# Performance work log

Measured on AMD Instinct MI355X. Metric: run time of the kernel, lower is better.

The kernel has to match this reference:

```python
import jax, jax.numpy as jnp
import numpy as np

N, D_IN, N_CTRS, D_OUT = 65536, 64, 1024, 256


def setup_inputs() -> dict:
    key = jax.random.key(0)
    k_x, k_c, k_v = jax.random.split(key, 3)
    x = jax.random.normal(k_x, (N, D_IN), dtype=jnp.float32)
    # learned params: centers (init_ctrs 'random' draws from data scale), values (normal), scales s=ones
    ctrs = jax.random.normal(k_c, (N_CTRS, D_IN), dtype=jnp.float32)
    values = jax.random.normal(k_v, (N_CTRS, D_OUT), dtype=jnp.float32) * 1e-2
    s = jnp.ones((D_IN,), dtype=jnp.float32)
    return {"x": x, "ctrs": ctrs, "values": values, "s": s}


def reference(x, ctrs, values, s):
    # dist_sq[n,k] = sum_d (x[n,d]-ctrs[k,d])^2 * s[d]
    # expanded to avoid the (N, n_ctrs, d_in) broadcast intermediate:
    x_sq = jnp.einsum('nd,d->n', x * x, s)            # (N,)
    c_sq = jnp.einsum('kd,d->k', ctrs * ctrs, s)      # (K,)
    cross = jnp.einsum('nd,kd->nk', x * s, ctrs)      # (N, K)
    dist_sq = x_sq[:, None] + c_sq[None, :] - 2.0 * cross
    assignments = jax.nn.softmax(-dist_sq, axis=1)    # (N, K)
    return assignments @ values                        # (N, d_out)
```

## Files before the change

### kernel.cpp

```cpp
#include <hip/hip_runtime.h>

typedef _Float16 half_t;
typedef half_t f16x8 __attribute__((ext_vector_type(8)));
typedef float f32x4 __attribute__((ext_vector_type(4)));
typedef unsigned int u32x2 __attribute__((ext_vector_type(2)));

#define LOG2E 1.44269504088896340736f

#define NROWS 65536
#define DIN   64
#define NCTRS 1024
#define DOUT  256

#define CSWZ_OFF 0
#define CSWZ_BYTES (128 * 1024)
#define VSWZ_OFF (CSWZ_OFF + CSWZ_BYTES)
#define VSWZ_BYTES (512 * 1024)
#define CSQ_OFF  (VSWZ_OFF + VSWZ_BYTES)

#define VT_STRIDE 260
#define CT_STRIDE 68

#define RESCALE_THR 8.0f

#define GLOAD_LDS16(g, l)                                                      \
  __builtin_amdgcn_global_load_lds(                                            \
      (const __attribute__((address_space(1))) void*)(const void*)(g),         \
      (__attribute__((address_space(3))) void*)(void*)(l), 16, 0, 0)

__global__ __launch_bounds__(256) void precompute_kernel(
    const float* __restrict__ ctrs, const float* __restrict__ values,
    const float* __restrict__ s, char* __restrict__ ws) {
  half_t* Cswz = (half_t*)(ws + CSWZ_OFF);
  half_t* Vswz = (half_t*)(ws + VSWZ_OFF);
  float* csq2 = (float*)(ws + CSQ_OFF);

  __shared__ half_t Vt[32 * VT_STRIDE];
  __shared__ half_t Ct[32 * CT_STRIDE];

  const int c = blockIdx.x, tid = threadIdx.x;

#pragma unroll
  for (int i = 0; i < 8; ++i) {
    int idx = i * 256 + tid;
    int r = idx >> 6, c4 = (idx & 63) * 4;
    float4 v = ((const float4*)values)[(size_t)(c * 32 + r) * 64 + (idx & 63)];
    Vt[r * VT_STRIDE + c4 + 0] = (half_t)v.x;
    Vt[r * VT_STRIDE + c4 + 1] = (half_t)v.y;
    Vt[r * VT_STRIDE + c4 + 2] = (half_t)v.z;
    Vt[r * VT_STRIDE + c4 + 3] = (half_t)v.w;
  }
#pragma unroll
  for (int i = 0; i < 2; ++i) {
    int idx = i * 256 + tid;
    int r = idx >> 4, c4 = (idx & 15) * 4;
    float4 v = ((const float4*)ctrs)[(size_t)(c * 32 + r) * 16 + (idx & 15)];
    Ct[r * CT_STRIDE + c4 + 0] = (half_t)v.x;
    Ct[r * CT_STRIDE + c4 + 1] = (half_t)v.y;
    Ct[r * CT_STRIDE + c4 + 2] = (half_t)v.z;
    Ct[r * CT_STRIDE + c4 + 3] = (half_t)v.w;
  }
  {
    int k = tid >> 3, dg = (tid & 7) * 8;
    const float* cp = ctrs + (size_t)(c * 32 + k) * DIN + dg;
    float acc = 0.0f;
#pragma unroll
    for (int j = 0; j < 8; ++j) acc = fmaf(cp[j] * cp[j], s[dg + j], acc);
    acc += __shfl_xor(acc, 1);
    acc += __shfl_xor(acc, 2);
    acc += __shfl_xor(acc, 4);
    if ((tid & 7) == 0) csq2[c * 32 + k] = acc * LOG2E;
  }
  __syncthreads();

  const int w = tid >> 6, l = tid & 63, l4 = l >> 4, lm = l & 15;

  {
    int ct = w >> 1, kt = w & 1;
    f16x8 v;
#pragma unroll
    for (int j = 0; j < 8; ++j)
      v[j] = Ct[(ct * 16 + lm) * CT_STRIDE + kt * 32 + l4 * 8 + j];
    *(f16x8*)(Cswz + ((c * 4 + w) * 64 + l) * 8) = v;
  }
#pragma unroll
  for (int q = 0; q < 4; ++q) {
    int sl = w * 4 + q;
    f16x8 v;
#pragma unroll
    for (int j = 0; j < 8; ++j)
      v[j] = Vt[(l4 * 8 + j) * VT_STRIDE + sl * 16 + lm];
    *(f16x8*)(Vswz + ((c * 16 + sl) * 64 + l) * 8) = v;
  }
}

__global__ __launch_bounds__(256, 2) void attn_kernel(
    const float* __restrict__ x, const float* __restrict__ s,
    const char* __restrict__ ws, float* __restrict__ out) {
  const f16x8* cbase = (const f16x8*)(ws + CSWZ_OFF);
  const char* Vraw = ws + VSWZ_OFF;
  const float* csq2 = (const float*)(ws + CSQ_OFF);

  __shared__ __attribute__((aligned(16))) char vbuf[2][16384];

  const int tid = threadIdx.x;
  const int w = tid >> 6, l = tid & 63, l4 = l >> 4, lm = l & 15;
  const int rowbase = blockIdx.x * 128 + w * 32;

#pragma unroll
  for (int i = 0; i < 4; ++i) {
    GLOAD_LDS16(Vraw + i * 4096 + tid * 16, &vbuf[0][i * 4096 + w * 1024]);
  }

  f16x8 A[2][2];
#pragma unroll
  for (int rt = 0; rt < 2; ++rt) {
#pragma unroll
    for (int kt = 0; kt < 2; ++kt) {
      int din = kt * 32 + l4 * 8;
      const float* src = x + (rowbase + rt * 16 + lm) * DIN + din;
      f16x8 a;
#pragma unroll
      for (int j = 0; j < 8; ++j) a[j] = (half_t)(src[j] * s[din + j]);
      A[rt][kt] = a;
    }
  }

  f16x8 ones;
#pragma unroll
  for (int j = 0; j < 8; ++j) ones[j] = (lm == 0) ? (half_t)1.0f : (half_t)0.0f;

  f32x4 O[2][16];
  f32x4 Lacc[2];
  float m[2] = {-1e30f, -1e30f};
#pragma unroll
  for (int rt = 0; rt < 2; ++rt) {
    Lacc[rt] = (f32x4){0.f, 0.f, 0.f, 0.f};
#pragma unroll
    for (int u = 0; u < 16; ++u) O[rt][u] = (f32x4){0.f, 0.f, 0.f, 0.f};
  }

#pragma unroll 1
  for (int c = 0; c < 32; ++c) {
    const int cur = c & 1;
    asm volatile("s_waitcnt vmcnt(0)" ::: "memory");
    __builtin_amdgcn_s_barrier();
    __builtin_amdgcn_sched_barrier(0);

    f16x8 b0 = cbase[(c * 4 + 0) * 64 + l];
    f16x8 b1 = cbase[(c * 4 + 1) * 64 + l];
    f16x8 b2 = cbase[(c * 4 + 2) * 64 + l];
    f16x8 b3 = cbase[(c * 4 + 3) * 64 + l];
    f32x4 cs0 = *(const f32x4*)(csq2 + c * 32 + l4 * 4);
    f32x4 cs1 = *(const f32x4*)(csq2 + c * 32 + 16 + l4 * 4);
    __builtin_amdgcn_sched_barrier(0);

    if (c < 31) {
      const char* src = Vraw + (size_t)(c + 1) * 16384;
#pragma unroll
      for (int i = 0; i < 4; ++i) {
        GLOAD_LDS16(src + i * 4096 + tid * 16,
                    &vbuf[cur ^ 1][i * 4096 + w * 1024]);
      }
    }
    __builtin_amdgcn_sched_barrier(0);

    f16x8 pb[2];
#pragma unroll
    for (int rt = 0; rt < 2; ++rt) {
      f32x4 t0 = {0.f, 0.f, 0.f, 0.f}, t1 = {0.f, 0.f, 0.f, 0.f};
      t0 = __builtin_amdgcn_mfma_f32_16x16x32_f16(b0, A[rt][0], t0, 0, 0, 0);
      t0 = __builtin_amdgcn_mfma_f32_16x16x32_f16(b1, A[rt][1], t0, 0, 0, 0);
      t1 = __builtin_amdgcn_mfma_f32_16x16x32_f16(b2, A[rt][0], t1, 0, 0, 0);
      t1 = __builtin_amdgcn_mfma_f32_16x16x32_f16(b3, A[rt][1], t1, 0, 0, 0);

      float v0[4], v1[4];
      float pm = -1e30f;
#pragma unroll
      for (int j = 0; j < 4; ++j) {
        v0[j] = fmaf(t0[j], 2.0f * LOG2E, -cs0[j]);
        v1[j] = fmaf(t1[j], 2.0f * LOG2E, -cs1[j]);
        pm = fmaxf(pm, fmaxf(v0[j], v1[j]));
      }
      pm = fmaxf(pm, __shfl_xor(pm, 16));
      pm = fmaxf(pm, __shfl_xor(pm, 32));

      if (__any(pm > m[rt] + RESCALE_THR)) {
        float mn = fmaxf(m[rt], pm);
        float f = __builtin_amdgcn_exp2f(m[rt] - mn);
        m[rt] = mn;
        Lacc[rt] *= f;
#pragma unroll
        for (int u = 0; u < 16; ++u) O[rt][u] *= f;
      }

      unsigned wds[4];
#pragma unroll
      for (int h = 0; h < 2; ++h) {
        union { half_t h2[2]; unsigned u; } qa, qb;
        qa.h2[0] = (half_t)__builtin_amdgcn_exp2f(v0[2 * h] - m[rt]);
        qa.h2[1] = (half_t)__builtin_amdgcn_exp2f(v0[2 * h + 1] - m[rt]);
        qb.h2[0] = (half_t)__builtin_amdgcn_exp2f(v1[2 * h] - m[rt]);
        qb.h2[1] = (half_t)__builtin_amdgcn_exp2f(v1[2 * h + 1] - m[rt]);
        u32x2 sw1 = __builtin_amdgcn_permlane32_swap(qa.u, qb.u, false, false);
        u32x2 sw2 = __builtin_amdgcn_permlane16_swap(sw1.x, sw1.y, false, false);
        wds[h] = sw2.x;
        wds[h + 2] = sw2.y;
      }
      union { unsigned u[4]; f16x8 v; } pk;
      pk.u[0] = wds[0]; pk.u[1] = wds[1]; pk.u[2] = wds[2]; pk.u[3] = wds[3];
      pb[rt] = pk.v;
    }

    const char* vb = &vbuf[cur][l * 16];
#pragma unroll
    for (int u = 0; u < 16; ++u) {
      f16x8 vf = *(const f16x8*)(vb + u * 1024);
      O[0][u] = __builtin_amdgcn_mfma_f32_16x16x32_f16(vf, pb[0], O[0][u], 0, 0, 0);
      O[1][u] = __builtin_amdgcn_mfma_f32_16x16x32_f16(vf, pb[1], O[1][u], 0, 0, 0);
    }
    Lacc[0] = __builtin_amdgcn_mfma_f32_16x16x32_f16(ones, pb[0], Lacc[0], 0, 0, 0);
    Lacc[1] = __builtin_amdgcn_mfma_f32_16x16x32_f16(ones, pb[1], Lacc[1], 0, 0, 0);
  }

#pragma unroll
  for (int rt = 0; rt < 2; ++rt) {
    float lv = __shfl(Lacc[rt][0], lm);
    float inv = 1.0f / fmaxf(lv, 1e-30f);
    float* po = out + (size_t)(rowbase + rt * 16 + lm) * DOUT + l4 * 4;
#pragma unroll
    for (int u = 0; u < 16; ++u) {
      f32x4 ov = O[rt][u] * inv;
      *(f32x4*)(po + u * 16) = ov;
    }
  }
}

extern "C" void kernel_launch(void* const* d_in, const int* in_sizes, int n_in,
                              void* d_out, int out_size, void* d_ws, size_t ws_size,
                              hipStream_t stream) {
  const float* x = (const float*)d_in[0];
  const float* ctrs = (const float*)d_in[1];
  const float* values = (const float*)d_in[2];
  const float* s = (const float*)d_in[3];
  float* out = (float*)d_out;
  char* ws = (char*)d_ws;

  hipLaunchKernelGGL(precompute_kernel, dim3(32), dim3(256), 0, stream,
                     ctrs, values, s, ws);
  hipLaunchKernelGGL(attn_kernel, dim3(512), dim3(256), 0, stream,
                     x, s, ws, out);
}
```

Before: 142.4 us.

## Halve rows per wave and triple-buffer value tiles with deeper prefetch

Each wave now handles 16 rows instead of 32, so twice as many blocks are launched and accumulator registers are halved, which allows three blocks per CU. The value-tile LDS buffer moves from double to triple buffering with a two-chunk-ahead prefetch and a partial vmcnt wait, so global-to-LDS copies overlap more with compute. The cost is that every value tile loaded into LDS is reused by half as many rows, which doubles total V and center traffic. The last iterations also issue redundant clamped prefetches.

```diff
diff --git a/kernel.cpp b/kernel.cpp
--- a/kernel.cpp
+++ b/kernel.cpp
@@ -94,56 +94,57 @@
   }
 }
 
-__global__ __launch_bounds__(256, 2) void attn_kernel(
+__global__ __launch_bounds__(256, 3) void attn_kernel(
     const float* __restrict__ x, const float* __restrict__ s,
     const char* __restrict__ ws, float* __restrict__ out) {
   const f16x8* cbase = (const f16x8*)(ws + CSWZ_OFF);
   const char* Vraw = ws + VSWZ_OFF;
   const float* csq2 = (const float*)(ws + CSQ_OFF);
 
-  __shared__ __attribute__((aligned(16))) char vbuf[2][16384];
+  __shared__ __attribute__((aligned(16))) char vbuf[3][16384];
 
   const int tid = threadIdx.x;
   const int w = tid >> 6, l = tid & 63, l4 = l >> 4, lm = l & 15;
-  const int rowbase = blockIdx.x * 128 + w * 32;
-
-#pragma unroll
-  for (int i = 0; i < 4; ++i) {
+  const int rowbase = blockIdx.x * 64 + w * 16;
+
+#pragma unroll
+  for (int i = 0; i < 4; ++i)
     GLOAD_LDS16(Vraw + i * 4096 + tid * 16, &vbuf[0][i * 4096 + w * 1024]);
-  }
-
-  f16x8 A[2][2];
-#pragma unroll
-  for (int rt = 0; rt < 2; ++rt) {
-#pragma unroll
-    for (int kt = 0; kt < 2; ++kt) {
-      int din = kt * 32 + l4 * 8;
-      const float* src = x + (rowbase + rt * 16 + lm) * DIN + din;
-      f16x8 a;
-#pragma unroll
-      for (int j = 0; j < 8; ++j) a[j] = (half_t)(src[j] * s[din + j]);
-      A[rt][kt] = a;
-    }
+  __builtin_amdgcn_sched_barrier(0);
+
+  f16x8 A[2];
+#pragma unroll
+  for (int kt = 0; kt < 2; ++kt) {
+    int din = kt * 32 + l4 * 8;
+    const float* src = x + (size_t)(rowbase + lm) * DIN + din;
+    f16x8 a;
+#pragma unroll
+    for (int j = 0; j < 8; ++j) a[j] = (half_t)(src[j] * s[din + j]);
+    A[kt] = a;
   }
 
   f16x8 ones;
 #pragma unroll
   for (int j = 0; j < 8; ++j) ones[j] = (lm == 0) ? (half_t)1.0f : (half_t)0.0f;
 
-  f32x4 O[2][16];
-  f32x4 Lacc[2];
-  float m[2] = {-1e30f, -1e30f};
-#pragma unroll
-  for (int rt = 0; rt < 2; ++rt) {
-    Lacc[rt] = (f32x4){0.f, 0.f, 0.f, 0.f};
-#pragma unroll
-    for (int u = 0; u < 16; ++u) O[rt][u] = (f32x4){0.f, 0.f, 0.f, 0.f};
-  }
-
+  __builtin_amdgcn_sched_barrier(0);
+#pragma unroll
+  for (int i = 0; i < 4; ++i)
+    GLOAD_LDS16(Vraw + 16384 + i * 4096 + tid * 16,
+                &vbuf[1][i * 4096 + w * 1024]);
+  __builtin_amdgcn_sched_barrier(0);
+
+  f32x4 O[16];
+  f32x4 Lacc;
+  float m = -1e30f;
+  Lacc = (f32x4){0.f, 0.f, 0.f, 0.f};
+#pragma unroll
+  for (int u = 0; u < 16; ++u) O[u] = (f32x4){0.f, 0.f, 0.f, 0.f};
+
+  int cur = 0;
 #pragma unroll 1
   for (int c = 0; c < 32; ++c) {
-    const int cur = c & 1;
-    asm volatile("s_waitcnt vmcnt(0)" ::: "memory");
+    asm volatile("s_waitcnt vmcnt(4)" ::: "memory");
     __builtin_amdgcn_s_barrier();
     __builtin_amdgcn_sched_barrier(0);
 
@@ -155,82 +156,78 @@
     f32x4 cs1 = *(const f32x4*)(csq2 + c * 32 + 16 + l4 * 4);
     __builtin_amdgcn_sched_barrier(0);
 
-    if (c < 31) {
-      const char* src = Vraw + (size_t)(c + 1) * 16384;
-#pragma unroll
-      for (int i = 0; i < 4; ++i) {
-        GLOAD_LDS16(src + i * 4096 + tid * 16,
-                    &vbuf[cur ^ 1][i * 4096 + w * 1024]);
-      }
+    {
+      int cn = (c + 2 < 32) ? c + 2 : 31;
+      int bn = cur + 2;
+      if (bn >= 3) bn -= 3;
+      const char* src = Vraw + (size_t)cn * 16384;
+#pragma unroll
+      for (int i = 0; i < 4; ++i)
+        GLOAD_LDS16(src + i * 4096 + tid * 16, &vbuf[bn][i * 4096 + w * 1024]);
     }
     __builtin_amdgcn_sched_barrier(0);
 
-    f16x8 pb[2];
-#pragma unroll
-    for (int rt = 0; rt < 2; ++rt) {
-      f32x4 t0 = {0.f, 0.f, 0.f, 0.f}, t1 = {0.f, 0.f, 0.f, 0.f};
-      t0 = __builtin_amdgcn_mfma_f32_16x16x32_f16(b0, A[rt][0], t0, 0, 0, 0);
-      t0 = __builtin_amdgcn_mfma_f32_16x16x32_f16(b1, A[rt][1], t0, 0, 0, 0);
-      t1 = __builtin_amdgcn_mfma_f32_16x16x32_f16(b2, A[rt][0], t1, 0, 0, 0);
-      t1 = __builtin_amdgcn_mfma_f32_16x16x32_f16(b3, A[rt][1], t1, 0, 0, 0);
-
-      float v0[4], v1[4];
-      float pm = -1e30f;
-#pragma unroll
-      for (int j = 0; j < 4; ++j) {
-        v0[j] = fmaf(t0[j], 2.0f * LOG2E, -cs0[j]);
-        v1[j] = fmaf(t1[j], 2.0f * LOG2E, -cs1[j]);
-        pm = fmaxf(pm, fmaxf(v0[j], v1[j]));
-      }
-      pm = fmaxf(pm, __shfl_xor(pm, 16));
-      pm = fmaxf(pm, __shfl_xor(pm, 32));
-
-      if (__any(pm > m[rt] + RESCALE_THR)) {
-        float mn = fmaxf(m[rt], pm);
-        float f = __builtin_amdgcn_exp2f(m[rt] - mn);
-        m[rt] = mn;
-        Lacc[rt] *= f;
-#pragma unroll
-        for (int u = 0; u < 16; ++u) O[rt][u] *= f;
-      }
-
-      unsigned wds[4];
-#pragma unroll
-      for (int h = 0; h < 2; ++h) {
-        union { half_t h2[2]; unsigned u; } qa, qb;
-        qa.h2[0] = (half_t)__builtin_amdgcn_exp2f(v0[2 * h] - m[rt]);
-        qa.h2[1] = (half_t)__builtin_amdgcn_exp2f(v0[2 * h + 1] - m[rt]);
-        qb.h2[0] = (half_t)__builtin_amdgcn_exp2f(v1[2 * h] - m[rt]);
-        qb.h2[1] = (half_t)__builtin_amdgcn_exp2f(v1[2 * h + 1] - m[rt]);
-        u32x2 sw1 = __builtin_amdgcn_permlane32_swap(qa.u, qb.u, false, false);
-        u32x2 sw2 = __builtin_amdgcn_permlane16_swap(sw1.x, sw1.y, false, false);
-        wds[h] = sw2.x;
-        wds[h + 2] = sw2.y;
-      }
-      union { unsigned u[4]; f16x8 v; } pk;
-      pk.u[0] = wds[0]; pk.u[1] = wds[1]; pk.u[2] = wds[2]; pk.u[3] = wds[3];
-      pb[rt] = pk.v;
-    }
+    f32x4 t0 = {0.f, 0.f, 0.f, 0.f}, t1 = {0.f, 0.f, 0.f, 0.f};
+    t0 = __builtin_amdgcn_mfma_f32_16x16x32_f16(b0, A[0], t0, 0, 0, 0);
+    t0 = __builtin_amdgcn_mfma_f32_16x16x32_f16(b1, A[1], t0, 0, 0, 0);
+    t1 = __builtin_amdgcn_mfma_f32_16x16x32_f16(b2, A[0], t1, 0, 0, 0);
+    t1 = __builtin_amdgcn_mfma_f32_16x16x32_f16(b3, A[1], t1, 0, 0, 0);
+
+    float v0[4], v1[4];
+    float pm = -1e30f;
+#pragma unroll
+    for (int j = 0; j < 4; ++j) {
+      v0[j] = fmaf(t0[j], 2.0f * LOG2E, -cs0[j]);
+      v1[j] = fmaf(t1[j], 2.0f * LOG2E, -cs1[j]);
+      pm = fmaxf(pm, fmaxf(v0[j], v1[j]));
+    }
+    pm = fmaxf(pm, __shfl_xor(pm, 16));
+    pm = fmaxf(pm, __shfl_xor(pm, 32));
+
+    if (__any(pm > m + RESCALE_THR)) {
+      float mn = fmaxf(m, pm);
+      float f = __builtin_amdgcn_exp2f(m - mn);
+      m = mn;
+      Lacc *= f;
+#pragma unroll
+      for (int u = 0; u < 16; ++u) O[u] *= f;
+    }
+
+    unsigned wds[4];
+#pragma unroll
+    for (int h = 0; h < 2; ++h) {
+      union { half_t h2[2]; unsigned u; } qa, qb;
+      qa.h2[0] = (half_t)__builtin_amdgcn_exp2f(v0[2 * h] - m);
+      qa.h2[1] = (half_t)__builtin_amdgcn_exp2f(v0[2 * h + 1] - m);
+      qb.h2[0] = (half_t)__builtin_amdgcn_exp2f(v1[2 * h] - m);
+      qb.h2[1] = (half_t)__builtin_amdgcn_exp2f(v1[2 * h + 1] - m);
+      u32x2 sw1 = __builtin_amdgcn_permlane32_swap(qa.u, qb.u, false, false);
+      u32x2 sw2 = __builtin_amdgcn_permlane16_swap(sw1.x, sw1.y, false, false);
+      wds[h] = sw2.x;
+      wds[h + 2] = sw2.y;
+    }
+    union { unsigned u[4]; f16x8 v; } pk;
+    pk.u[0] = wds[0]; pk.u[1] = wds[1]; pk.u[2] = wds[2]; pk.u[3] = wds[3];
+    f16x8 pb = pk.v;
 
     const char* vb = &vbuf[cur][l * 16];
 #pragma unroll
     for (int u = 0; u < 16; ++u) {
       f16x8 vf = *(const f16x8*)(vb + u * 1024);
-      O[0][u] = __builtin_amdgcn_mfma_f32_16x16x32_f16(vf, pb[0], O[0][u], 0, 0, 0);
-      O[1][u] = __builtin_amdgcn_mfma_f32_16x16x32_f16(vf, pb[1], O[1][u], 0, 0, 0);
-    }
-    Lacc[0] = __builtin_amdgcn_mfma_f32_16x16x32_f16(ones, pb[0], Lacc[0], 0, 0, 0);
-    Lacc[1] = __builtin_amdgcn_mfma_f32_16x16x32_f16(ones, pb[1], Lacc[1], 0, 0, 0);
-  }
-
-#pragma unroll
-  for (int rt = 0; rt < 2; ++rt) {
-    float lv = __shfl(Lacc[rt][0], lm);
+      O[u] = __builtin_amdgcn_mfma_f32_16x16x32_f16(vf, pb, O[u], 0, 0, 0);
+    }
+    Lacc = __builtin_amdgcn_mfma_f32_16x16x32_f16(ones, pb, Lacc, 0, 0, 0);
+
+    cur = (cur == 2) ? 0 : cur + 1;
+  }
+
+  {
+    float lv = __shfl(Lacc[0], lm);
     float inv = 1.0f / fmaxf(lv, 1e-30f);
-    float* po = out + (size_t)(rowbase + rt * 16 + lm) * DOUT + l4 * 4;
+    float* po = out + (size_t)(rowbase + lm) * DOUT + l4 * 4;
 #pragma unroll
     for (int u = 0; u < 16; ++u) {
-      f32x4 ov = O[rt][u] * inv;
+      f32x4 ov = O[u] * inv;
       *(f32x4*)(po + u * 16) = ov;
     }
   }
@@ -248,6 +245,6 @@
 
   hipLaunchKernelGGL(precompute_kernel, dim3(32), dim3(256), 0, stream,
                      ctrs, values, s, ws);
-  hipLaunchKernelGGL(attn_kernel, dim3(512), dim3(256), 0, stream,
+  hipLaunchKernelGGL(attn_kernel, dim3(1024), dim3(256), 0, stream,
                      x, s, ws, out);
 }
```

Result: slower. 157.3 us (+10.4%).

## Software-pipeline score MFMAs, stage centers/csq in LDS, triple-buffer values, widen precompute

Applied to the files above, without the earlier changes.

The attention kernel now computes the next chunk's distance MFMAs while the current chunk's softmax and value MFMAs run, so QK work overlaps the PV accumulation. Center tiles and csq are staged into LDS via global_load_lds instead of being read from global memory each iteration. Value tiles are triple-buffered with a partial vmcnt wait, and the PV MFMAs get raised priority through setprio. The precompute kernel is split across 256 blocks instead of 32. Together these add LDS use (about 68KB per block) and extra register pressure from the carried score tiles, which risks lower occupancy.

```diff
diff --git a/kernel.cpp b/kernel.cpp
--- a/kernel.cpp
+++ b/kernel.cpp
@@ -18,7 +18,6 @@
 #define VSWZ_BYTES (512 * 1024)
 #define CSQ_OFF  (VSWZ_OFF + VSWZ_BYTES)
 
-#define VT_STRIDE 260
 #define CT_STRIDE 68
 
 #define RESCALE_THR 8.0f
@@ -35,47 +34,53 @@
   half_t* Vswz = (half_t*)(ws + VSWZ_OFF);
   float* csq2 = (float*)(ws + CSQ_OFF);
 
-  __shared__ half_t Vt[32 * VT_STRIDE];
+  __shared__ half_t Vt[32 * 36];
   __shared__ half_t Ct[32 * CT_STRIDE];
 
-  const int c = blockIdx.x, tid = threadIdx.x;
-
-#pragma unroll
-  for (int i = 0; i < 8; ++i) {
-    int idx = i * 256 + tid;
-    int r = idx >> 6, c4 = (idx & 63) * 4;
-    float4 v = ((const float4*)values)[(size_t)(c * 32 + r) * 64 + (idx & 63)];
-    Vt[r * VT_STRIDE + c4 + 0] = (half_t)v.x;
-    Vt[r * VT_STRIDE + c4 + 1] = (half_t)v.y;
-    Vt[r * VT_STRIDE + c4 + 2] = (half_t)v.z;
-    Vt[r * VT_STRIDE + c4 + 3] = (half_t)v.w;
-  }
-#pragma unroll
-  for (int i = 0; i < 2; ++i) {
-    int idx = i * 256 + tid;
-    int r = idx >> 4, c4 = (idx & 15) * 4;
-    float4 v = ((const float4*)ctrs)[(size_t)(c * 32 + r) * 16 + (idx & 15)];
-    Ct[r * CT_STRIDE + c4 + 0] = (half_t)v.x;
-    Ct[r * CT_STRIDE + c4 + 1] = (half_t)v.y;
-    Ct[r * CT_STRIDE + c4 + 2] = (half_t)v.z;
-    Ct[r * CT_STRIDE + c4 + 3] = (half_t)v.w;
-  }
+  const int bid = blockIdx.x, tid = threadIdx.x;
+  const int c = bid & 31, part = bid >> 5;
+  const int w = tid >> 6, l = tid & 63, l4 = l >> 4, lm = l & 15;
+
   {
-    int k = tid >> 3, dg = (tid & 7) * 8;
-    const float* cp = ctrs + (size_t)(c * 32 + k) * DIN + dg;
-    float acc = 0.0f;
-#pragma unroll
-    for (int j = 0; j < 8; ++j) acc = fmaf(cp[j] * cp[j], s[dg + j], acc);
-    acc += __shfl_xor(acc, 1);
-    acc += __shfl_xor(acc, 2);
-    acc += __shfl_xor(acc, 4);
-    if ((tid & 7) == 0) csq2[c * 32 + k] = acc * LOG2E;
+    int r = tid >> 3, f4 = tid & 7;
+    float4 v = ((const float4*)values)[(size_t)(c * 32 + r) * 64 + part * 8 + f4];
+    half_t* d = Vt + r * 36 + f4 * 4;
+    d[0] = (half_t)v.x; d[1] = (half_t)v.y;
+    d[2] = (half_t)v.z; d[3] = (half_t)v.w;
+  }
+  if (part == 0) {
+#pragma unroll
+    for (int i = 0; i < 2; ++i) {
+      int idx = i * 256 + tid;
+      int r = idx >> 4, c4 = (idx & 15) * 4;
+      float4 v = ((const float4*)ctrs)[(size_t)(c * 32 + r) * 16 + (idx & 15)];
+      Ct[r * CT_STRIDE + c4 + 0] = (half_t)v.x;
+      Ct[r * CT_STRIDE + c4 + 1] = (half_t)v.y;
+      Ct[r * CT_STRIDE + c4 + 2] = (half_t)v.z;
+      Ct[r * CT_STRIDE + c4 + 3] = (half_t)v.w;
+    }
+    {
+      int k = tid >> 3, dg = (tid & 7) * 8;
+      const float* cp = ctrs + (size_t)(c * 32 + k) * DIN + dg;
+      float acc = 0.0f;
+#pragma unroll
+      for (int j = 0; j < 8; ++j) acc = fmaf(cp[j] * cp[j], s[dg + j], acc);
+      acc += __shfl_xor(acc, 1);
+      acc += __shfl_xor(acc, 2);
+      acc += __shfl_xor(acc, 4);
+      if ((tid & 7) == 0) csq2[c * 32 + k] = acc * LOG2E;
+    }
   }
   __syncthreads();
 
-  const int w = tid >> 6, l = tid & 63, l4 = l >> 4, lm = l & 15;
-
-  {
+  if (w < 2) {
+    int sl = part * 2 + w;
+    f16x8 v;
+#pragma unroll
+    for (int j = 0; j < 8; ++j) v[j] = Vt[(l4 * 8 + j) * 36 + w * 16 + lm];
+    *(f16x8*)(Vswz + ((c * 16 + sl) * 64 + l) * 8) = v;
+  }
+  if (part == 0) {
     int ct = w >> 1, kt = w & 1;
     f16x8 v;
 #pragma unroll
@@ -83,34 +88,39 @@
       v[j] = Ct[(ct * 16 + lm) * CT_STRIDE + kt * 32 + l4 * 8 + j];
     *(f16x8*)(Cswz + ((c * 4 + w) * 64 + l) * 8) = v;
   }
-#pragma unroll
-  for (int q = 0; q < 4; ++q) {
-    int sl = w * 4 + q;
-    f16x8 v;
-#pragma unroll
-    for (int j = 0; j < 8; ++j)
-      v[j] = Vt[(l4 * 8 + j) * VT_STRIDE + sl * 16 + lm];
-    *(f16x8*)(Vswz + ((c * 16 + sl) * 64 + l) * 8) = v;
-  }
 }
 
 __global__ __launch_bounds__(256, 2) void attn_kernel(
     const float* __restrict__ x, const float* __restrict__ s,
     const char* __restrict__ ws, float* __restrict__ out) {
-  const f16x8* cbase = (const f16x8*)(ws + CSWZ_OFF);
+  const char* Craw = ws + CSWZ_OFF;
   const char* Vraw = ws + VSWZ_OFF;
-  const float* csq2 = (const float*)(ws + CSQ_OFF);
-
-  __shared__ __attribute__((aligned(16))) char vbuf[2][16384];
+  const char* csqg = ws + CSQ_OFF;
+
+  __shared__ __attribute__((aligned(16))) char vbuf[3][16384];
+  __shared__ __attribute__((aligned(16))) char cbuf[4][4096];
+  __shared__ __attribute__((aligned(16))) float csq_l[1024];
 
   const int tid = threadIdx.x;
   const int w = tid >> 6, l = tid & 63, l4 = l >> 4, lm = l & 15;
   const int rowbase = blockIdx.x * 128 + w * 32;
 
-#pragma unroll
-  for (int i = 0; i < 4; ++i) {
-    GLOAD_LDS16(Vraw + i * 4096 + tid * 16, &vbuf[0][i * 4096 + w * 1024]);
-  }
+#define STAGE_V(chunk, bufidx)                                                 \
+  do {                                                                         \
+    const char* _s = Vraw + (size_t)(chunk) * 16384;                           \
+    char* _d = vbuf[bufidx];                                                   \
+    _Pragma("unroll") for (int _i = 0; _i < 4; ++_i)                           \
+        GLOAD_LDS16(_s + _i * 4096 + tid * 16, _d + _i * 4096 + w * 1024);     \
+  } while (0)
+#define STAGE_C(chunk, bufidx)                                                 \
+  GLOAD_LDS16(Craw + (size_t)(chunk) * 4096 + tid * 16,                        \
+              (char*)cbuf[bufidx] + w * 1024)
+
+  STAGE_V(0, 0);
+  STAGE_C(0, 0);
+  STAGE_C(1, 1);
+  GLOAD_LDS16(csqg + tid * 16, (char*)csq_l + w * 1024);
+  __builtin_amdgcn_sched_barrier(0);
 
   f16x8 A[2][2];
 #pragma unroll
@@ -118,7 +128,7 @@
 #pragma unroll
     for (int kt = 0; kt < 2; ++kt) {
       int din = kt * 32 + l4 * 8;
-      const float* src = x + (rowbase + rt * 16 + lm) * DIN + din;
+      const float* src = x + (size_t)(rowbase + rt * 16 + lm) * DIN + din;
       f16x8 a;
 #pragma unroll
       for (int j = 0; j < 8; ++j) a[j] = (half_t)(src[j] * s[din + j]);
@@ -129,6 +139,31 @@
   f16x8 ones;
 #pragma unroll
   for (int j = 0; j < 8; ++j) ones[j] = (lm == 0) ? (half_t)1.0f : (half_t)0.0f;
+
+  __syncthreads();
+
+  f32x4 t[2][2];
+  {
+    const char* cb = cbuf[0];
+    f16x8 b0 = *(const f16x8*)(cb + 0 * 1024 + l * 16);
+    f16x8 b1 = *(const f16x8*)(cb + 1 * 1024 + l * 16);
+    f16x8 b2 = *(const f16x8*)(cb + 2 * 1024 + l * 16);
+    f16x8 b3 = *(const f16x8*)(cb + 3 * 1024 + l * 16);
+#pragma unroll
+    for (int rt = 0; rt < 2; ++rt) {
+      f32x4 a0 = {0.f, 0.f, 0.f, 0.f}, a1 = {0.f, 0.f, 0.f, 0.f};
+      a0 = __builtin_amdgcn_mfma_f32_16x16x32_f16(b0, A[rt][0], a0, 0, 0, 0);
+      a0 = __builtin_amdgcn_mfma_f32_16x16x32_f16(b1, A[rt][1], a0, 0, 0, 0);
+      a1 = __builtin_amdgcn_mfma_f32_16x16x32_f16(b2, A[rt][0], a1, 0, 0, 0);
+      a1 = __builtin_amdgcn_mfma_f32_16x16x32_f16(b3, A[rt][1], a1, 0, 0, 0);
+      t[rt][0] = a0;
+      t[rt][1] = a1;
+    }
+  }
+  __builtin_amdgcn_sched_barrier(0);
+  STAGE_V(1, 1);
+  STAGE_C(2, 2);
+  __builtin_amdgcn_sched_barrier(0);
 
   f32x4 O[2][16];
   f32x4 Lacc[2];
@@ -140,48 +175,42 @@
     for (int u = 0; u < 16; ++u) O[rt][u] = (f32x4){0.f, 0.f, 0.f, 0.f};
   }
 
+  int vcur = 0;
 #pragma unroll 1
   for (int c = 0; c < 32; ++c) {
-    const int cur = c & 1;
-    asm volatile("s_waitcnt vmcnt(0)" ::: "memory");
+    asm volatile("s_waitcnt vmcnt(5)" ::: "memory");
     __builtin_amdgcn_s_barrier();
     __builtin_amdgcn_sched_barrier(0);
 
-    f16x8 b0 = cbase[(c * 4 + 0) * 64 + l];
-    f16x8 b1 = cbase[(c * 4 + 1) * 64 + l];
-    f16x8 b2 = cbase[(c * 4 + 2) * 64 + l];
-    f16x8 b3 = cbase[(c * 4 + 3) * 64 + l];
-    f32x4 cs0 = *(const f32x4*)(csq2 + c * 32 + l4 * 4);
-    f32x4 cs1 = *(const f32x4*)(csq2 + c * 32 + 16 + l4 * 4);
+    {
+      int vn = (c + 2 < 32) ? c + 2 : 31;
+      int cn = (c + 3 < 32) ? c + 3 : 31;
+      int vnb = vcur + 2;
+      if (vnb >= 3) vnb -= 3;
+      STAGE_V(vn, vnb);
+      STAGE_C(cn, (c + 3) & 3);
+    }
     __builtin_amdgcn_sched_barrier(0);
 
-    if (c < 31) {
-      const char* src = Vraw + (size_t)(c + 1) * 16384;
-#pragma unroll
-      for (int i = 0; i < 4; ++i) {
-        GLOAD_LDS16(src + i * 4096 + tid * 16,
-                    &vbuf[cur ^ 1][i * 4096 + w * 1024]);
+    const char* cb = cbuf[(c + 1) & 3];
+    f16x8 b0 = *(const f16x8*)(cb + 0 * 1024 + l * 16);
+    f16x8 b1 = *(const f16x8*)(cb + 1 * 1024 + l * 16);
+    f16x8 b2 = *(const f16x8*)(cb + 2 * 1024 + l * 16);
+    f16x8 b3 = *(const f16x8*)(cb + 3 * 1024 + l * 16);
+    f32x4 cs0 = *(const f32x4*)&csq_l[c * 32 + l4 * 4];
+    f32x4 cs1 = *(const f32x4*)&csq_l[c * 32 + 16 + l4 * 4];
+
+    f16x8 pb[2];
+#pragma unroll
+    for (int rt = 0; rt < 2; ++rt) {
+      float v0[4], v1[4];
+#pragma unroll
+      for (int j = 0; j < 4; ++j) {
+        v0[j] = fmaf(t[rt][0][j], 2.0f * LOG2E, -cs0[j]);
+        v1[j] = fmaf(t[rt][1][j], 2.0f * LOG2E, -cs1[j]);
       }
-    }
-    __builtin_amdgcn_sched_barrier(0);
-
-    f16x8 pb[2];
-#pragma unroll
-    for (int rt = 0; rt < 2; ++rt) {
-      f32x4 t0 = {0.f, 0.f, 0.f, 0.f}, t1 = {0.f, 0.f, 0.f, 0.f};
-      t0 = __builtin_amdgcn_mfma_f32_16x16x32_f16(b0, A[rt][0], t0, 0, 0, 0);
-      t0 = __builtin_amdgcn_mfma_f32_16x16x32_f16(b1, A[rt][1], t0, 0, 0, 0);
-      t1 = __builtin_amdgcn_mfma_f32_16x16x32_f16(b2, A[rt][0], t1, 0, 0, 0);
-      t1 = __builtin_amdgcn_mfma_f32_16x16x32_f16(b3, A[rt][1], t1, 0, 0, 0);
-
-      float v0[4], v1[4];
-      float pm = -1e30f;
-#pragma unroll
-      for (int j = 0; j < 4; ++j) {
-        v0[j] = fmaf(t0[j], 2.0f * LOG2E, -cs0[j]);
-        v1[j] = fmaf(t1[j], 2.0f * LOG2E, -cs1[j]);
-        pm = fmaxf(pm, fmaxf(v0[j], v1[j]));
-      }
+      float pm = fmaxf(fmaxf(fmaxf(v0[0], v0[1]), fmaxf(v0[2], v0[3])),
+                       fmaxf(fmaxf(v1[0], v1[1]), fmaxf(v1[2], v1[3])));
       pm = fmaxf(pm, __shfl_xor(pm, 16));
       pm = fmaxf(pm, __shfl_xor(pm, 32));
 
@@ -212,7 +241,19 @@
       pb[rt] = pk.v;
     }
 
-    const char* vb = &vbuf[cur][l * 16];
+#pragma unroll
+    for (int rt = 0; rt < 2; ++rt) {
+      f32x4 a0 = {0.f, 0.f, 0.f, 0.f}, a1 = {0.f, 0.f, 0.f, 0.f};
+      a0 = __builtin_amdgcn_mfma_f32_16x16x32_f16(b0, A[rt][0], a0, 0, 0, 0);
+      a0 = __builtin_amdgcn_mfma_f32_16x16x32_f16(b1, A[rt][1], a0, 0, 0, 0);
+      a1 = __builtin_amdgcn_mfma_f32_16x16x32_f16(b2, A[rt][0], a1, 0, 0, 0);
+      a1 = __builtin_amdgcn_mfma_f32_16x16x32_f16(b3, A[rt][1], a1, 0, 0, 0);
+      t[rt][0] = a0;
+      t[rt][1] = a1;
+    }
+
+    __builtin_amdgcn_s_setprio(1);
+    const char* vb = &vbuf[vcur][l * 16];
 #pragma unroll
     for (int u = 0; u < 16; ++u) {
       f16x8 vf = *(const f16x8*)(vb + u * 1024);
@@ -221,6 +262,9 @@
     }
     Lacc[0] = __builtin_amdgcn_mfma_f32_16x16x32_f16(ones, pb[0], Lacc[0], 0, 0, 0);
     Lacc[1] = __builtin_amdgcn_mfma_f32_16x16x32_f16(ones, pb[1], Lacc[1], 0, 0, 0);
+    __builtin_amdgcn_s_setprio(0);
+
+    vcur = (vcur == 2) ? 0 : vcur + 1;
   }
 
 #pragma unroll
@@ -234,6 +278,8 @@
       *(f32x4*)(po + u * 16) = ov;
     }
   }
+#undef STAGE_V
+#undef STAGE_C
 }
 
 extern "C" void kernel_launch(void* const* d_in, const int* in_sizes, int n_in,
@@ -246,7 +292,7 @@
   float* out = (float*)d_out;
   char* ws = (char*)d_ws;
 
-  hipLaunchKernelGGL(precompute_kernel, dim3(32), dim3(256), 0, stream,
+  hipLaunchKernelGGL(precompute_kernel, dim3(256), dim3(256), 0, stream,
                      ctrs, values, s, ws);
   hipLaunchKernelGGL(attn_kernel, dim3(512), dim3(256), 0, stream,
                      x, s, ws, out);
```

Result: no change. 141.1 us (-0.9%).
